# Kernel optimization log

Hardware: AMD Instinct MI355X
Metric: run time of the kernel (lower is better)

## Reference

```python
import jax, jax.numpy as jnp
import numpy as np

# Module config (init_kwargs)
OUT_H, OUT_W = 7, 7
SPATIAL_SCALE = 0.25
SAMPLE_NUM = 2          # fixed sampling grid (sample_num > 0 branch of mmcv kernel)
ALIGNED = True
CLOCKWISE = False

B, C, H, W = 2, 256, 200, 200
R = 1000


def setup_inputs() -> dict:
    key = jax.random.key(0)
    k1, k2, k3, k4, k5, k6 = jax.random.split(key, 6)
    features = jax.random.normal(k1, (B, C, H, W), dtype=jnp.float32)
    # rois: (batch_index, cx, cy, w, h, angle) in input-image coordinates
    bidx = jax.random.randint(k2, (R,), 0, B).astype(jnp.float32)
    cx = jax.random.uniform(k3, (R,), minval=100.0, maxval=700.0)
    cy = jax.random.uniform(k4, (R,), minval=100.0, maxval=700.0)
    wh = jax.random.uniform(k5, (R, 2), minval=20.0, maxval=200.0)
    ang = jax.random.uniform(k6, (R,), minval=-np.pi, maxval=np.pi)
    rois = jnp.concatenate(
        [bidx[:, None], cx[:, None], cy[:, None], wh, ang[:, None]], axis=1
    ).astype(jnp.float32)
    return {"features": features, "rois": rois}


def _bilinear_gather(features, bidx, y, x):
    """features: [B,C,H,W]; bidx: [R] int; y,x: [R,P] float. Returns [R,P,C]."""
    Hf, Wf = features.shape[2], features.shape[3]
    valid = (y > -1.0) & (y < Hf) & (x > -1.0) & (x < Wf)
    y = jnp.maximum(y, 0.0)
    x = jnp.maximum(x, 0.0)
    yl = jnp.floor(y).astype(jnp.int32)
    xl = jnp.floor(x).astype(jnp.int32)
    ych = yl >= Hf - 1
    xch = xl >= Wf - 1
    yl = jnp.where(ych, Hf - 1, yl)
    yh = jnp.where(ych, Hf - 1, yl + 1)
    xl = jnp.where(xch, Wf - 1, xl)
    xh = jnp.where(xch, Wf - 1, xl + 1)
    ly = jnp.where(ych, 0.0, y - yl.astype(y.dtype))
    lx = jnp.where(xch, 0.0, x - xl.astype(x.dtype))
    hy, hx = 1.0 - ly, 1.0 - lx
    b = bidx[:, None]  # [R,1] broadcast against [R,P]
    v1 = features[b, :, yl, xl]  # [R,P,C]
    v2 = features[b, :, yl, xh]
    v3 = features[b, :, yh, xl]
    v4 = features[b, :, yh, xh]
    val = (hy * hx)[..., None] * v1 + (hy * lx)[..., None] * v2 \
        + (ly * hx)[..., None] * v3 + (ly * lx)[..., None] * v4
    return jnp.where(valid[..., None], val, 0.0)


def _roi_align_rotated(features, rois):
    g = SAMPLE_NUM
    offset = 0.5 if ALIGNED else 0.0
    bidx = rois[:, 0].astype(jnp.int32)
    cx = rois[:, 1] * SPATIAL_SCALE - offset
    cy = rois[:, 2] * SPATIAL_SCALE - offset
    rw = rois[:, 3] * SPATIAL_SCALE
    rh = rois[:, 4] * SPATIAL_SCALE
    theta = -rois[:, 5] if CLOCKWISE else rois[:, 5]
    if not ALIGNED:
        rw = jnp.maximum(rw, 1.0)
        rh = jnp.maximum(rh, 1.0)
    bin_h = rh / OUT_H
    bin_w = rw / OUT_W
    # sample offsets within roi frame, origin at roi center
    ph = jnp.arange(OUT_H, dtype=jnp.float32)
    pw = jnp.arange(OUT_W, dtype=jnp.float32)
    ig = (jnp.arange(g, dtype=jnp.float32) + 0.5) / g
    # yy: [R, OUT_H, g]; xx: [R, OUT_W, g]
    yy = -rh[:, None, None] / 2.0 + (ph[None, :, None] + ig[None, None, :]) * bin_h[:, None, None]
    xx = -rw[:, None, None] / 2.0 + (pw[None, :, None] + ig[None, None, :]) * bin_w[:, None, None]
    # broadcast to [R, OUT_H, OUT_W, g, g]
    yy5 = yy[:, :, None, :, None]
    xx5 = xx[:, None, :, None, :]
    sin_t = jnp.sin(theta)[:, None, None, None, None]
    cos_t = jnp.cos(theta)[:, None, None, None, None]
    x = yy5 * sin_t + xx5 * cos_t + cx[:, None, None, None, None]
    y = yy5 * cos_t - xx5 * sin_t + cy[:, None, None, None, None]
    P = OUT_H * OUT_W * g * g
    vals = _bilinear_gather(features, bidx, y.reshape(R, P), x.reshape(R, P))  # [R,P,C]
    vals = vals.reshape(R, OUT_H, OUT_W, g * g, C).mean(axis=3)  # [R,OUT_H,OUT_W,C]
    return jnp.transpose(vals, (0, 3, 1, 2))  # [R,C,OUT_H,OUT_W]


def reference(features, rois):
    return _roi_align_rotated(features, rois)
```

## Files before the change

### kernel.cpp

```cpp
#include <hip/hip_runtime.h>
#include <math.h>

#define OUT_H 7
#define OUT_W 7
#define GS 2
#define NBINS (OUT_H * OUT_W)
#define NSAMP (GS * GS)
#define SPATIAL_SCALE 0.25f
#define B_ 2
#define C_ 256
#define H_ 200
#define W_ 200
#define R_ 1000
#define HW_ (H_ * W_)
#define NBH 25

typedef _Float16 half_t;
typedef __attribute__((ext_vector_type(4))) _Float16 half4;
typedef __attribute__((ext_vector_type(2))) _Float16 half2_t;


__global__ __launch_bounds__(1024)
void build_perm(const float* __restrict__ rois, int* __restrict__ perm) {
    __shared__ int cnt[8];
    __shared__ int novf, take;
    __shared__ unsigned char claimed[R_];
    __shared__ short ovf[R_];
    const int t = threadIdx.x;
    if (t < 8) cnt[t] = 0;
    if (t == 0) { novf = 0; take = 0; }
    if (t < R_) claimed[t] = 0;
    __syncthreads();
    if (t < R_) {
        const float* roi = rois + t * 6;
        int   b   = (int)roi[0];
        float cyf = roi[2] * SPATIAL_SCALE;
        int q = (int)((cyf - 25.0f) * (4.0f / 150.0f));
        q = q < 0 ? 0 : (q > 3 ? 3 : q);
        int band = b * 4 + q;
        band = band < 0 ? 0 : (band > 7 ? 7 : band);
        int rank = atomicAdd(&cnt[band], 1);
        if (rank < R_ / 8) {
            int id = band + 8 * rank;
            perm[id] = t;
            claimed[id] = 1;
        } else {
            ovf[atomicAdd(&novf, 1)] = (short)t;
        }
    }
    __syncthreads();
    if (t < R_ && !claimed[t]) {
        perm[t] = (int)ovf[atomicAdd(&take, 1)];
    }
}

__global__ __launch_bounds__(256)
void nchw_to_nhwc_h(const float* __restrict__ in, half_t* __restrict__ out) {
    __shared__ float tile[64][65];
    const int hw0 = blockIdx.x * 64;
    const int c0  = blockIdx.y * 64;
    const int b   = blockIdx.z;

    {
        const int tx = threadIdx.x & 63;
        const int ty = threadIdx.x >> 6;
        const float* ip = in + ((size_t)b * C_ + c0) * HW_ + hw0;
#pragma unroll
        for (int k = 0; k < 16; ++k)
            tile[ty + 4 * k][tx] = ip[(size_t)(ty + 4 * k) * HW_ + tx];
    }
    __syncthreads();
    {
        const int cp = threadIdx.x & 31;
        const int hr = threadIdx.x >> 5;
        half_t* op = out + ((size_t)b * HW_ + hw0) * C_ + c0;
#pragma unroll
        for (int k = 0; k < 8; ++k) {
            const int hw = hr + 8 * k;
            half2_t h;
            h[0] = (half_t)tile[2 * cp + 0][hw];
            h[1] = (half_t)tile[2 * cp + 1][hw];
            ((half2_t*)(op + (size_t)hw * C_))[cp] = h;
        }
    }
}

template<int B0, int NB>
__device__ __forceinline__ void gather_pass(
        const half4* __restrict__ fp, int bplane,
        float cx, float cy, float rw, float rh,
        float st, float ct, float bin_h, float bin_w,
        int wave, int lane, int tid,
        float (&obuf)[4][64][NBH], float* __restrict__ out_r) {

    for (int j = wave; j < NB; j += 8) {
        const int bin = B0 + j;
        const int ph = bin / OUT_W, pw = bin % OUT_W;
        float accx = 0.0f, accy = 0.0f, accz = 0.0f, accw = 0.0f;

#pragma unroll
        for (int s = 0; s < NSAMP; ++s) {
            const int iy = s >> 1, ix = s & 1;
            const float yy = -rh * 0.5f + ((float)ph + ((float)iy + 0.5f) * 0.5f) * bin_h;
            const float xx = -rw * 0.5f + ((float)pw + ((float)ix + 0.5f) * 0.5f) * bin_w;
            float x = yy * st + xx * ct + cx;
            float y = yy * ct - xx * st + cy;

            const bool valid = (y > -1.0f) && (y < (float)H_) &&
                               (x > -1.0f) && (x < (float)W_);
            y = fmaxf(y, 0.0f);
            x = fmaxf(x, 0.0f);
            int yl = (int)y, xl = (int)x;
            int yh; float ly;
            if (yl >= H_ - 1) { yl = H_ - 1; yh = H_ - 1; ly = 0.0f; }
            else              { yh = yl + 1; ly = y - (float)yl; }
            int xh; float lx;
            if (xl >= W_ - 1) { xl = W_ - 1; xh = W_ - 1; lx = 0.0f; }
            else              { xh = xl + 1; lx = x - (float)xl; }
            const float hy = 1.0f - ly, hx = 1.0f - lx;
            const float scale = valid ? (1.0f / NSAMP) : 0.0f;
            const float w0 = hy * hx * scale, w1 = hy * lx * scale;
            const float w2 = ly * hx * scale, w3 = ly * lx * scale;

            const int p0 = bplane + yl * W_ + xl;
            const int p1 = bplane + yl * W_ + xh;
            const int p2 = bplane + yh * W_ + xl;
            const int p3 = bplane + yh * W_ + xh;

            const half4 v0 = fp[p0 * (C_ / 4) + lane];
            const half4 v1 = fp[p1 * (C_ / 4) + lane];
            const half4 v2 = fp[p2 * (C_ / 4) + lane];
            const half4 v3 = fp[p3 * (C_ / 4) + lane];

            accx += w0 * (float)v0[0] + w1 * (float)v1[0] + w2 * (float)v2[0] + w3 * (float)v3[0];
            accy += w0 * (float)v0[1] + w1 * (float)v1[1] + w2 * (float)v2[1] + w3 * (float)v3[1];
            accz += w0 * (float)v0[2] + w1 * (float)v1[2] + w2 * (float)v2[2] + w3 * (float)v3[2];
            accw += w0 * (float)v0[3] + w1 * (float)v1[3] + w2 * (float)v2[3] + w3 * (float)v3[3];
        }

        obuf[0][lane][j] = accx;
        obuf[1][lane][j] = accy;
        obuf[2][lane][j] = accz;
        obuf[3][lane][j] = accw;
    }
    __syncthreads();

    const int E = C_ * NB;
#pragma unroll
    for (int i = 0; i < (E + 511) / 512; ++i) {
        const int e = tid + 512 * i;
        if (e < E) {
            const int c = e / NB;
            const int j = e - c * NB;
            out_r[(size_t)c * NBINS + B0 + j] = obuf[c & 3][c >> 2][j];
        }
    }
    __syncthreads();
}

__global__ __launch_bounds__(512)
void gather_nhwc(const half_t* __restrict__ nhwc,
                 const float* __restrict__ rois,
                 const int* __restrict__ perm,
                 float* __restrict__ out) {
    __shared__ float obuf[4][64][NBH];

    const int r    = perm[blockIdx.x];
    const int wave = threadIdx.x >> 6;
    const int lane = threadIdx.x & 63;

    const float* roi = rois + r * 6;
    const int   b     = (int)roi[0];
    const float cx    = roi[1] * SPATIAL_SCALE - 0.5f;
    const float cy    = roi[2] * SPATIAL_SCALE - 0.5f;
    const float rw    = roi[3] * SPATIAL_SCALE;
    const float rh    = roi[4] * SPATIAL_SCALE;
    const float theta = roi[5];
    const float bin_h = rh * (1.0f / OUT_H);
    const float bin_w = rw * (1.0f / OUT_W);
    float st, ct;
    __sincosf(theta, &st, &ct);

    const int bplane = b * HW_;
    const half4* __restrict__ fp = (const half4*)nhwc;
    float* out_r = out + (size_t)r * (C_ * NBINS);

    gather_pass< 0, 25>(fp, bplane, cx, cy, rw, rh, st, ct, bin_h, bin_w,
                        wave, lane, (int)threadIdx.x, obuf, out_r);
    gather_pass<25, 24>(fp, bplane, cx, cy, rw, rh, st, ct, bin_h, bin_w,
                        wave, lane, (int)threadIdx.x, obuf, out_r);
}


struct alignas(16) Samp {
    int o0, o1, o2, o3;
    float w0, w1, w2, w3;
};

__device__ __forceinline__ Samp compute_samp(const float* __restrict__ rois,
                                             int r, int ph, int pw, int s) {
    const float* roi = rois + r * 6;
    int   b     = (int)roi[0];
    float cx    = roi[1] * SPATIAL_SCALE - 0.5f;
    float cy    = roi[2] * SPATIAL_SCALE - 0.5f;
    float rw    = roi[3] * SPATIAL_SCALE;
    float rh    = roi[4] * SPATIAL_SCALE;
    float theta = roi[5];
    float bin_h = rh * (1.0f / OUT_H);
    float bin_w = rw * (1.0f / OUT_W);
    int iy = s / GS, ix = s % GS;
    float yy = -rh * 0.5f + ((float)ph + ((float)iy + 0.5f) * (1.0f / GS)) * bin_h;
    float xx = -rw * 0.5f + ((float)pw + ((float)ix + 0.5f) * (1.0f / GS)) * bin_w;
    float st = sinf(theta), ct = cosf(theta);
    float x = yy * st + xx * ct + cx;
    float y = yy * ct - xx * st + cy;
    bool valid = (y > -1.0f) && (y < (float)H_) && (x > -1.0f) && (x < (float)W_);
    y = fmaxf(y, 0.0f);
    x = fmaxf(x, 0.0f);
    int yl = (int)y;
    int xl = (int)x;
    int yh; float ly;
    if (yl >= H_ - 1) { yl = H_ - 1; yh = H_ - 1; ly = 0.0f; }
    else              { yh = yl + 1; ly = y - (float)yl; }
    int xh; float lx;
    if (xl >= W_ - 1) { xl = W_ - 1; xh = W_ - 1; lx = 0.0f; }
    else              { xh = xl + 1; lx = x - (float)xl; }
    float hy = 1.0f - ly, hx = 1.0f - lx;
    float scale = valid ? (1.0f / NSAMP) : 0.0f;
    Samp sp;
    int base = b * (C_ * H_ * W_);
    sp.o0 = base + yl * W_ + xl;
    sp.o1 = base + yl * W_ + xh;
    sp.o2 = base + yh * W_ + xl;
    sp.o3 = base + yh * W_ + xh;
    sp.w0 = hy * hx * scale;
    sp.w1 = hy * lx * scale;
    sp.w2 = ly * hx * scale;
    sp.w3 = ly * lx * scale;
    return sp;
}

__global__ __launch_bounds__(256)
void mono_kernel(const float* __restrict__ feat,
                 const float* __restrict__ rois,
                 float* __restrict__ out) {
    int tid = blockIdx.x * blockDim.x + threadIdx.x;
    if (tid >= R_ * C_ * NBINS) return;
    int bin = tid % NBINS;
    int rc  = tid / NBINS;
    int c   = rc % C_;
    int r   = rc / C_;
    int coff = c * (H_ * W_);
    float acc = 0.0f;
#pragma unroll
    for (int s = 0; s < NSAMP; ++s) {
        Samp t = compute_samp(rois, r, bin / OUT_W, bin % OUT_W, s);
        acc += t.w0 * feat[coff + t.o0];
        acc += t.w1 * feat[coff + t.o1];
        acc += t.w2 * feat[coff + t.o2];
        acc += t.w3 * feat[coff + t.o3];
    }
    out[tid] = acc;
}


extern "C" void kernel_launch(void* const* d_in, const int* in_sizes, int n_in,
                              void* d_out, int out_size, void* d_ws, size_t ws_size,
                              hipStream_t stream) {
    const float* feat = (const float*)d_in[0];
    const float* rois = (const float*)d_in[1];
    float* out = (float*)d_out;

    const size_t nhwc_bytes = (size_t)B_ * C_ * HW_ * sizeof(half_t);
    const size_t perm_bytes = (size_t)R_ * sizeof(int);

    if (ws_size >= nhwc_bytes + perm_bytes) {
        half_t* nhwc = (half_t*)d_ws;
        int*    perm = (int*)((char*)d_ws + nhwc_bytes);
        build_perm<<<1, 1024, 0, stream>>>(rois, perm);
        dim3 tgrid(HW_ / 64, C_ / 64, B_);
        nchw_to_nhwc_h<<<tgrid, 256, 0, stream>>>(feat, nhwc);
        gather_nhwc<<<R_, 512, 0, stream>>>(nhwc, rois, perm, out);
    } else {
        const int n_out = R_ * C_ * NBINS;
        mono_kernel<<<(n_out + 255) / 256, 256, 0, stream>>>(feat, rois, out);
    }
}
```

Baseline: 180.5 us.

## Fuse ROI permutation into transpose and precompute sample metadata in LDS

The ROI-permutation kernel is folded into the first block of the NCHW-to-NHWC transpose kernel, which removes one launch. In the gather kernel, the 196 per-sample bilinear offsets and weights are computed once by separate threads into shared memory. This replaces the redundant per-wave coordinate math, and the inner loop now issues eight independent half4 loads before its FMAs. It costs extra LDS per block and a block-wide sync, and block 0 of the transpose now carries serial permutation work. A launch-bounds occupancy hint is also added.

```diff
diff --git a/kernel.cpp b/kernel.cpp
--- a/kernel.cpp
+++ b/kernel.cpp
@@ -6,6 +6,7 @@
 #define GS 2
 #define NBINS (OUT_H * OUT_W)
 #define NSAMP (GS * GS)
+#define NMETA (NBINS * NSAMP)
 #define SPATIAL_SCALE 0.25f
 #define B_ 2
 #define C_ 256
@@ -20,43 +21,44 @@
 typedef __attribute__((ext_vector_type(2))) _Float16 half2_t;
 
 
-__global__ __launch_bounds__(1024)
-void build_perm(const float* __restrict__ rois, int* __restrict__ perm) {
+__global__ __launch_bounds__(256)
+void nchw_to_nhwc_h(const float* __restrict__ in, half_t* __restrict__ out,
+                    const float* __restrict__ rois, int* __restrict__ perm) {
+    __shared__ float tile[64][65];
+
     __shared__ int cnt[8];
     __shared__ int novf, take;
     __shared__ unsigned char claimed[R_];
     __shared__ short ovf[R_];
-    const int t = threadIdx.x;
-    if (t < 8) cnt[t] = 0;
-    if (t == 0) { novf = 0; take = 0; }
-    if (t < R_) claimed[t] = 0;
-    __syncthreads();
-    if (t < R_) {
-        const float* roi = rois + t * 6;
-        int   b   = (int)roi[0];
-        float cyf = roi[2] * SPATIAL_SCALE;
-        int q = (int)((cyf - 25.0f) * (4.0f / 150.0f));
-        q = q < 0 ? 0 : (q > 3 ? 3 : q);
-        int band = b * 4 + q;
-        band = band < 0 ? 0 : (band > 7 ? 7 : band);
-        int rank = atomicAdd(&cnt[band], 1);
-        if (rank < R_ / 8) {
-            int id = band + 8 * rank;
-            perm[id] = t;
-            claimed[id] = 1;
-        } else {
-            ovf[atomicAdd(&novf, 1)] = (short)t;
-        }
-    }
-    __syncthreads();
-    if (t < R_ && !claimed[t]) {
-        perm[t] = (int)ovf[atomicAdd(&take, 1)];
-    }
-}
-
-__global__ __launch_bounds__(256)
-void nchw_to_nhwc_h(const float* __restrict__ in, half_t* __restrict__ out) {
-    __shared__ float tile[64][65];
+    if (blockIdx.x == 0 && blockIdx.y == 0 && blockIdx.z == 0) {
+        const int t0 = threadIdx.x;
+        if (t0 < 8) cnt[t0] = 0;
+        if (t0 == 0) { novf = 0; take = 0; }
+        for (int t = t0; t < R_; t += 256) claimed[t] = 0;
+        __syncthreads();
+        for (int t = t0; t < R_; t += 256) {
+            const float* roi = rois + t * 6;
+            int   b   = (int)roi[0];
+            float cyf = roi[2] * SPATIAL_SCALE;
+            int q = (int)((cyf - 25.0f) * (4.0f / 150.0f));
+            q = q < 0 ? 0 : (q > 3 ? 3 : q);
+            int band = b * 4 + q;
+            band = band < 0 ? 0 : (band > 7 ? 7 : band);
+            int rank = atomicAdd(&cnt[band], 1);
+            if (rank < R_ / 8) {
+                int id = band + 8 * rank;
+                perm[id] = t;
+                claimed[id] = 1;
+            } else {
+                ovf[atomicAdd(&novf, 1)] = (short)t;
+            }
+        }
+        __syncthreads();
+        for (int t = t0; t < R_; t += 256) {
+            if (!claimed[t]) perm[t] = (int)ovf[atomicAdd(&take, 1)];
+        }
+    }
+
     const int hw0 = blockIdx.x * 64;
     const int c0  = blockIdx.y * 64;
     const int b   = blockIdx.z;
@@ -87,61 +89,70 @@
 
 template<int B0, int NB>
 __device__ __forceinline__ void gather_pass(
-        const half4* __restrict__ fp, int bplane,
-        float cx, float cy, float rw, float rh,
-        float st, float ct, float bin_h, float bin_w,
+        const half4* __restrict__ fp,
+        const int4* __restrict__ s_o, const float4* __restrict__ s_w,
         int wave, int lane, int tid,
         float (&obuf)[4][64][NBH], float* __restrict__ out_r) {
 
     for (int j = wave; j < NB; j += 8) {
-        const int bin = B0 + j;
-        const int ph = bin / OUT_W, pw = bin % OUT_W;
-        float accx = 0.0f, accy = 0.0f, accz = 0.0f, accw = 0.0f;
-
-#pragma unroll
-        for (int s = 0; s < NSAMP; ++s) {
-            const int iy = s >> 1, ix = s & 1;
-            const float yy = -rh * 0.5f + ((float)ph + ((float)iy + 0.5f) * 0.5f) * bin_h;
-            const float xx = -rw * 0.5f + ((float)pw + ((float)ix + 0.5f) * 0.5f) * bin_w;
-            float x = yy * st + xx * ct + cx;
-            float y = yy * ct - xx * st + cy;
-
-            const bool valid = (y > -1.0f) && (y < (float)H_) &&
-                               (x > -1.0f) && (x < (float)W_);
-            y = fmaxf(y, 0.0f);
-            x = fmaxf(x, 0.0f);
-            int yl = (int)y, xl = (int)x;
-            int yh; float ly;
-            if (yl >= H_ - 1) { yl = H_ - 1; yh = H_ - 1; ly = 0.0f; }
-            else              { yh = yl + 1; ly = y - (float)yl; }
-            int xh; float lx;
-            if (xl >= W_ - 1) { xl = W_ - 1; xh = W_ - 1; lx = 0.0f; }
-            else              { xh = xl + 1; lx = x - (float)xl; }
-            const float hy = 1.0f - ly, hx = 1.0f - lx;
-            const float scale = valid ? (1.0f / NSAMP) : 0.0f;
-            const float w0 = hy * hx * scale, w1 = hy * lx * scale;
-            const float w2 = ly * hx * scale, w3 = ly * lx * scale;
-
-            const int p0 = bplane + yl * W_ + xl;
-            const int p1 = bplane + yl * W_ + xh;
-            const int p2 = bplane + yh * W_ + xl;
-            const int p3 = bplane + yh * W_ + xh;
-
-            const half4 v0 = fp[p0 * (C_ / 4) + lane];
-            const half4 v1 = fp[p1 * (C_ / 4) + lane];
-            const half4 v2 = fp[p2 * (C_ / 4) + lane];
-            const half4 v3 = fp[p3 * (C_ / 4) + lane];
-
-            accx += w0 * (float)v0[0] + w1 * (float)v1[0] + w2 * (float)v2[0] + w3 * (float)v3[0];
-            accy += w0 * (float)v0[1] + w1 * (float)v1[1] + w2 * (float)v2[1] + w3 * (float)v3[1];
-            accz += w0 * (float)v0[2] + w1 * (float)v1[2] + w2 * (float)v2[2] + w3 * (float)v3[2];
-            accw += w0 * (float)v0[3] + w1 * (float)v1[3] + w2 * (float)v2[3] + w3 * (float)v3[3];
-        }
-
-        obuf[0][lane][j] = accx;
-        obuf[1][lane][j] = accy;
-        obuf[2][lane][j] = accz;
-        obuf[3][lane][j] = accw;
+        const int m = (B0 + j) * NSAMP;
+        float ax = 0.0f, ay = 0.0f, az = 0.0f, aw = 0.0f;
+
+#pragma unroll
+        for (int sp = 0; sp < 2; ++sp) {
+            const int4   oA = s_o[m + 2 * sp + 0];
+            const int4   oB = s_o[m + 2 * sp + 1];
+            const float4 wA = s_w[m + 2 * sp + 0];
+            const float4 wB = s_w[m + 2 * sp + 1];
+
+            const half4 vA0 = fp[oA.x + lane];
+            const half4 vA1 = fp[oA.y + lane];
+            const half4 vA2 = fp[oA.z + lane];
+            const half4 vA3 = fp[oA.w + lane];
+            const half4 vB0 = fp[oB.x + lane];
+            const half4 vB1 = fp[oB.y + lane];
+            const half4 vB2 = fp[oB.z + lane];
+            const half4 vB3 = fp[oB.w + lane];
+
+            ax = fmaf((float)vA0[0], wA.x, ax);
+            ay = fmaf((float)vA0[1], wA.x, ay);
+            az = fmaf((float)vA0[2], wA.x, az);
+            aw = fmaf((float)vA0[3], wA.x, aw);
+            ax = fmaf((float)vA1[0], wA.y, ax);
+            ay = fmaf((float)vA1[1], wA.y, ay);
+            az = fmaf((float)vA1[2], wA.y, az);
+            aw = fmaf((float)vA1[3], wA.y, aw);
+            ax = fmaf((float)vA2[0], wA.z, ax);
+            ay = fmaf((float)vA2[1], wA.z, ay);
+            az = fmaf((float)vA2[2], wA.z, az);
+            aw = fmaf((float)vA2[3], wA.z, aw);
+            ax = fmaf((float)vA3[0], wA.w, ax);
+            ay = fmaf((float)vA3[1], wA.w, ay);
+            az = fmaf((float)vA3[2], wA.w, az);
+            aw = fmaf((float)vA3[3], wA.w, aw);
+
+            ax = fmaf((float)vB0[0], wB.x, ax);
+            ay = fmaf((float)vB0[1], wB.x, ay);
+            az = fmaf((float)vB0[2], wB.x, az);
+            aw = fmaf((float)vB0[3], wB.x, aw);
+            ax = fmaf((float)vB1[0], wB.y, ax);
+            ay = fmaf((float)vB1[1], wB.y, ay);
+            az = fmaf((float)vB1[2], wB.y, az);
+            aw = fmaf((float)vB1[3], wB.y, aw);
+            ax = fmaf((float)vB2[0], wB.z, ax);
+            ay = fmaf((float)vB2[1], wB.z, ay);
+            az = fmaf((float)vB2[2], wB.z, az);
+            aw = fmaf((float)vB2[3], wB.z, aw);
+            ax = fmaf((float)vB3[0], wB.w, ax);
+            ay = fmaf((float)vB3[1], wB.w, ay);
+            az = fmaf((float)vB3[2], wB.w, az);
+            aw = fmaf((float)vB3[3], wB.w, aw);
+        }
+
+        obuf[0][lane][j] = ax;
+        obuf[1][lane][j] = ay;
+        obuf[2][lane][j] = az;
+        obuf[3][lane][j] = aw;
     }
     __syncthreads();
 
@@ -158,37 +169,72 @@
     __syncthreads();
 }
 
-__global__ __launch_bounds__(512)
+__global__ __launch_bounds__(512, 8)
 void gather_nhwc(const half_t* __restrict__ nhwc,
                  const float* __restrict__ rois,
                  const int* __restrict__ perm,
                  float* __restrict__ out) {
     __shared__ float obuf[4][64][NBH];
+    __shared__ int4   s_o[NMETA];
+    __shared__ float4 s_w[NMETA];
 
     const int r    = perm[blockIdx.x];
-    const int wave = threadIdx.x >> 6;
-    const int lane = threadIdx.x & 63;
-
-    const float* roi = rois + r * 6;
-    const int   b     = (int)roi[0];
-    const float cx    = roi[1] * SPATIAL_SCALE - 0.5f;
-    const float cy    = roi[2] * SPATIAL_SCALE - 0.5f;
-    const float rw    = roi[3] * SPATIAL_SCALE;
-    const float rh    = roi[4] * SPATIAL_SCALE;
-    const float theta = roi[5];
-    const float bin_h = rh * (1.0f / OUT_H);
-    const float bin_w = rw * (1.0f / OUT_W);
-    float st, ct;
-    __sincosf(theta, &st, &ct);
-
-    const int bplane = b * HW_;
+    const int tid  = threadIdx.x;
+    const int wave = tid >> 6;
+    const int lane = tid & 63;
+
+    if (tid < NMETA) {
+        const float* roi = rois + r * 6;
+        const int   b     = (int)roi[0];
+        const float cx    = roi[1] * SPATIAL_SCALE - 0.5f;
+        const float cy    = roi[2] * SPATIAL_SCALE - 0.5f;
+        const float rw    = roi[3] * SPATIAL_SCALE;
+        const float rh    = roi[4] * SPATIAL_SCALE;
+        const float theta = roi[5];
+        const float bin_h = rh * (1.0f / OUT_H);
+        const float bin_w = rw * (1.0f / OUT_W);
+        float st, ct;
+        __sincosf(theta, &st, &ct);
+
+        const int bin = tid >> 2;
+        const int s   = tid & 3;
+        const int ph  = bin / OUT_W, pw = bin % OUT_W;
+        const int iy  = s >> 1,      ix = s & 1;
+
+        const float yy = -rh * 0.5f + ((float)ph + ((float)iy + 0.5f) * 0.5f) * bin_h;
+        const float xx = -rw * 0.5f + ((float)pw + ((float)ix + 0.5f) * 0.5f) * bin_w;
+        float x = yy * st + xx * ct + cx;
+        float y = yy * ct - xx * st + cy;
+
+        const bool valid = (y > -1.0f) && (y < (float)H_) &&
+                           (x > -1.0f) && (x < (float)W_);
+        y = fmaxf(y, 0.0f);
+        x = fmaxf(x, 0.0f);
+        int yl = (int)y, xl = (int)x;
+        int yh; float ly;
+        if (yl >= H_ - 1) { yl = H_ - 1; yh = H_ - 1; ly = 0.0f; }
+        else              { yh = yl + 1; ly = y - (float)yl; }
+        int xh; float lx;
+        if (xl >= W_ - 1) { xl = W_ - 1; xh = W_ - 1; lx = 0.0f; }
+        else              { xh = xl + 1; lx = x - (float)xl; }
+        const float hy = 1.0f - ly, hx = 1.0f - lx;
+        const float scale = valid ? (1.0f / NSAMP) : 0.0f;
+
+        const int bplane = b * HW_;
+        s_o[tid] = make_int4((bplane + yl * W_ + xl) * (C_ / 4),
+                             (bplane + yl * W_ + xh) * (C_ / 4),
+                             (bplane + yh * W_ + xl) * (C_ / 4),
+                             (bplane + yh * W_ + xh) * (C_ / 4));
+        s_w[tid] = make_float4(hy * hx * scale, hy * lx * scale,
+                               ly * hx * scale, ly * lx * scale);
+    }
+    __syncthreads();
+
     const half4* __restrict__ fp = (const half4*)nhwc;
     float* out_r = out + (size_t)r * (C_ * NBINS);
 
-    gather_pass< 0, 25>(fp, bplane, cx, cy, rw, rh, st, ct, bin_h, bin_w,
-                        wave, lane, (int)threadIdx.x, obuf, out_r);
-    gather_pass<25, 24>(fp, bplane, cx, cy, rw, rh, st, ct, bin_h, bin_w,
-                        wave, lane, (int)threadIdx.x, obuf, out_r);
+    gather_pass< 0, 25>(fp, s_o, s_w, wave, lane, tid, obuf, out_r);
+    gather_pass<25, 24>(fp, s_o, s_w, wave, lane, tid, obuf, out_r);
 }
 
 
@@ -277,9 +323,8 @@
     if (ws_size >= nhwc_bytes + perm_bytes) {
         half_t* nhwc = (half_t*)d_ws;
         int*    perm = (int*)((char*)d_ws + nhwc_bytes);
-        build_perm<<<1, 1024, 0, stream>>>(rois, perm);
         dim3 tgrid(HW_ / 64, C_ / 64, B_);
-        nchw_to_nhwc_h<<<tgrid, 256, 0, stream>>>(feat, nhwc);
+        nchw_to_nhwc_h<<<tgrid, 256, 0, stream>>>(feat, nhwc, rois, perm);
         gather_nhwc<<<R_, 512, 0, stream>>>(nhwc, rois, perm, out);
     } else {
         const int n_out = R_ * C_ * NBINS;
```

Result: no change. 178.3 us (-1.2%).
